# Performance work log

Measured on AMD Instinct MI355X. Metric: run time of the kernel, lower is better.

## Reference

```python
import jax, jax.numpy as jnp
import numpy as np

NUM_HEADS = 16


def setup_inputs() -> dict:
    key = jax.random.key(0)
    ks = jax.random.split(key, 7)
    B, S, D = 2, 2048, 1024
    return {
        "query": jax.random.normal(ks[0], (B, S, D), jnp.float32),
        "key": jax.random.normal(ks[1], (B, S, D), jnp.float32),
        "value": jax.random.normal(ks[2], (B, S, D), jnp.float32),
        "qk_w": jax.random.normal(ks[3], (2 * D, D), jnp.float32) * (D ** -0.5),
        "qk_b": jax.random.normal(ks[4], (2 * D,), jnp.float32) * 0.02,
        "out_w": jax.random.normal(ks[5], (D, D), jnp.float32) * (D ** -0.5),
        "out_b": jax.random.normal(ks[6], (D,), jnp.float32) * 0.02,
    }


def reference(query, key, value, qk_w, qk_b, out_w, out_b):
    # Hand-rolled multi-head attention with fused QK projection (both Q and K
    # come from `query`); `key` arg is unused (as in the source forward).
    B, S, D = query.shape
    H = NUM_HEADS
    dh = D // H
    scale = D ** -0.5  # source uses d_model**-0.5, not head_dim

    qk = query @ qk_w.T + qk_b                      # [B, S, 2D]
    qk = qk.reshape(B, S, 2, H, dh).transpose(2, 0, 3, 1, 4)  # [2, B, H, S, dh]
    q, k = qk[0], qk[1]                              # [B, H, S, dh]

    scores = jnp.einsum("bhqd,bhkd->bhqk", q, k) * scale  # [B, H, S, S]
    attn = jax.nn.softmax(scores, axis=-1)
    # dropout_p = 0.0 -> identity (eval mode)

    v = value.reshape(B, S, H, dh).transpose(0, 2, 1, 3)   # [B, H, S, dh]
    out = jnp.einsum("bhqk,bhkd->bhqd", attn, v)           # [B, H, S, dh]
    out = out.transpose(0, 2, 1, 3).reshape(B, S, D)       # merge heads
    return out @ out_w.T + out_b
```

## Files before the change

kernel.cpp:

```cpp
#include <hip/hip_runtime.h>
#include <hip/hip_bf16.h>
#include <stdint.h>

typedef __attribute__((ext_vector_type(8))) short bf16x8;
typedef __attribute__((ext_vector_type(4))) short bf16x4;
typedef __attribute__((ext_vector_type(4))) float f32x4;
typedef __attribute__((ext_vector_type(16))) float f32x16;

#define B_ 2
#define H_ 16
#define S_ 2048
#define D_ 1024
#define DH 64

__device__ __forceinline__ void gload_lds16(const void* g, void* l) {
  __builtin_amdgcn_global_load_lds((const __attribute__((address_space(1))) void*)g,
                                   (__attribute__((address_space(3))) void*)l, 16, 0, 0);
}

__device__ __forceinline__ float exp2_hw(float x) {
  float r;
  asm("v_exp_f32 %0, %1" : "=v"(r) : "v"(x));
  return r;
}

__device__ __forceinline__ uint32_t packbf2(float lo, float hi) {
  union { __hip_bfloat162 h; uint32_t u; } u;
  u.h = __float22bfloat162_rn(make_float2(lo, hi));
  return u.u;
}

__device__ __forceinline__ void pl32swap(uint32_t& a, uint32_t& b) {
  asm volatile("v_permlane32_swap_b32 %0, %1" : "+v"(a), "+v"(b));
}

__global__ void k_f2b(const float* __restrict__ in, __hip_bfloat16* __restrict__ out, int n8) {
  int i = blockIdx.x * blockDim.x + threadIdx.x;
  if (i >= n8) return;
  const float4* p = (const float4*)in + (size_t)i * 2;
  float4 a = p[0], b = p[1];
  union { bf16x8 v; __hip_bfloat16 h[8]; } u;
  u.h[0] = __float2bfloat16(a.x); u.h[1] = __float2bfloat16(a.y);
  u.h[2] = __float2bfloat16(a.z); u.h[3] = __float2bfloat16(a.w);
  u.h[4] = __float2bfloat16(b.x); u.h[5] = __float2bfloat16(b.y);
  u.h[6] = __float2bfloat16(b.z); u.h[7] = __float2bfloat16(b.w);
  *((bf16x8*)out + i) = u.v;
}

__global__ void k_vt(const float* __restrict__ v, __hip_bfloat16* __restrict__ vt) {
  __shared__ float tile[64][65];
  const int bh = blockIdx.y, b = bh >> 4, h = bh & 15;
  const int s0 = blockIdx.x * 64;
  const int t = threadIdx.x;
#pragma unroll
  for (int it = 0; it < 4; ++it) {
    const int r = it * 16 + (t >> 4);
    const int c = (t & 15) * 4;
    const float4 x = *(const float4*)(v + (size_t)(b * S_ + s0 + r) * D_ + h * DH + c);
    tile[r][c] = x.x; tile[r][c + 1] = x.y; tile[r][c + 2] = x.z; tile[r][c + 3] = x.w;
  }
  __syncthreads();
#pragma unroll
  for (int it = 0; it < 4; ++it) {
    const int d = it * 16 + (t >> 4);
    const int j = (t & 15) * 4;
    union { bf16x4 v4; __hip_bfloat16 e[4]; } u;
    u.e[0] = __float2bfloat16(tile[j][d]);
    u.e[1] = __float2bfloat16(tile[j + 1][d]);
    u.e[2] = __float2bfloat16(tile[j + 2][d]);
    u.e[3] = __float2bfloat16(tile[j + 3][d]);
    *(bf16x4*)(vt + (size_t)(bh * DH + d) * S_ + s0 + j) = u.v4;
  }
}

__device__ __forceinline__ void gemm_tile_128(
    const __hip_bfloat16* __restrict__ A, const __hip_bfloat16* __restrict__ Bm,
    int K, int m0, int n0, __hip_bfloat16* As, __hip_bfloat16* Bs, f32x4 acc[4][4]) {
  const int t = threadIdx.x;
  const int l = t & 63, w = t >> 6;
  const int wr = w >> 1, wc = w & 1;
  const int lr = l & 15, lc = l >> 4;
  const int srow = t >> 2;
  const int sbyte = ((t & 3) << 4) ^ ((srow & 3) << 4);
  const char* AsB = (const char*)As;
  const char* BsB = (const char*)Bs;
  const int aswz = (lc << 4) ^ ((lr & 3) << 4);
  const size_t rowK = (size_t)K;
  const __hip_bfloat16* gA0 = A + (size_t)(m0 + srow) * rowK + (sbyte >> 1);
  const __hip_bfloat16* gB0 = Bm + (size_t)(n0 + srow) * rowK + (sbyte >> 1);
  for (int k0 = 0; k0 < K; k0 += 32) {
    __syncthreads();
    gload_lds16(gA0 + k0, (void*)&As[t * 8]);
    gload_lds16(gA0 + 64 * rowK + k0, (void*)&As[(256 + t) * 8]);
    gload_lds16(gB0 + k0, (void*)&Bs[t * 8]);
    gload_lds16(gB0 + 64 * rowK + k0, (void*)&Bs[(256 + t) * 8]);
    __syncthreads();
    bf16x8 af[4], bfr[4];
#pragma unroll
    for (int i = 0; i < 4; ++i)
      af[i] = *(const bf16x8*)(AsB + (wr * 64 + i * 16 + lr) * 64 + aswz);
#pragma unroll
    for (int j = 0; j < 4; ++j)
      bfr[j] = *(const bf16x8*)(BsB + (wc * 64 + j * 16 + lr) * 64 + aswz);
#pragma unroll
    for (int i = 0; i < 4; ++i)
#pragma unroll
      for (int j = 0; j < 4; ++j)
        acc[i][j] = __builtin_amdgcn_mfma_f32_16x16x32_bf16(af[i], bfr[j], acc[i][j], 0, 0, 0);
  }
}

__global__ __launch_bounds__(256) void k_gemm_qk(
    const __hip_bfloat16* __restrict__ A, const __hip_bfloat16* __restrict__ Bm,
    const float* __restrict__ bias,
    __hip_bfloat16* __restrict__ Qh, __hip_bfloat16* __restrict__ Kh) {
  __shared__ __align__(16) __hip_bfloat16 As[128 * 32];
  __shared__ __align__(16) __hip_bfloat16 Bs[128 * 32];
  f32x4 acc[4][4] = {};
  const int m0 = blockIdx.x * 128, n0 = blockIdx.y * 128;
  gemm_tile_128(A, Bm, 1024, m0, n0, As, Bs, acc);
  const int t = threadIdx.x, l = t & 63, w = t >> 6;
  const int wr = w >> 1, wc = w & 1, lr = l & 15, lc = l >> 4;
#pragma unroll
  for (int j = 0; j < 4; ++j) {
    const int col = n0 + wc * 64 + j * 16 + lr;
    const float bv = bias[col];
    const int inK = col >> 10;
    const int hh = (col & 1023) >> 6, dd = col & 63;
    __hip_bfloat16* dst = inK ? Kh : Qh;
    const float sc = inK ? 1.0f : 0.045084220f;
#pragma unroll
    for (int i = 0; i < 4; ++i) {
#pragma unroll
      for (int r = 0; r < 4; ++r) {
        const int row = m0 + wr * 64 + i * 16 + lc * 4 + r;
        const int b = row >> 11, s = row & 2047;
        const float vv = (acc[i][j][r] + bv) * sc;
        dst[((size_t)(b * H_ + hh) * S_ + s) * DH + dd] = __float2bfloat16(vv);
      }
    }
  }
}

__global__ __launch_bounds__(256) void k_gemm_out(
    const __hip_bfloat16* __restrict__ A, const __hip_bfloat16* __restrict__ Bm,
    const float* __restrict__ bias, float* __restrict__ out) {
  __shared__ __align__(16) __hip_bfloat16 As[128 * 32];
  __shared__ __align__(16) __hip_bfloat16 Bs[128 * 32];
  f32x4 acc[4][4] = {};
  const int m0 = blockIdx.x * 128, n0 = blockIdx.y * 128;
  gemm_tile_128(A, Bm, 1024, m0, n0, As, Bs, acc);
  const int t = threadIdx.x, l = t & 63, w = t >> 6;
  const int wr = w >> 1, wc = w & 1, lr = l & 15, lc = l >> 4;
#pragma unroll
  for (int j = 0; j < 4; ++j) {
    const int col = n0 + wc * 64 + j * 16 + lr;
    const float bv = bias[col];
#pragma unroll
    for (int i = 0; i < 4; ++i) {
#pragma unroll
      for (int r = 0; r < 4; ++r) {
        const int row = m0 + wr * 64 + i * 16 + lc * 4 + r;
        out[(size_t)row * D_ + col] = acc[i][j][r] + bv;
      }
    }
  }
}

__global__ __launch_bounds__(256) void k_attn(
    const __hip_bfloat16* __restrict__ Qh, const __hip_bfloat16* __restrict__ Kh,
    const __hip_bfloat16* __restrict__ VT, __hip_bfloat16* __restrict__ attO) {
  __shared__ __align__(16) __hip_bfloat16 KV[2][8192];
  __shared__ float fbuf[4][32];
  const int bh = blockIdx.y, q0 = blockIdx.x * 128;
  const int t = threadIdx.x, l = t & 63, w = t >> 6;
  const int qi = l & 31, hi = l >> 5;
  const __hip_bfloat16* Qb = Qh + (size_t)bh * S_ * DH;
  const __hip_bfloat16* Kb = Kh + (size_t)bh * S_ * DH;
  const __hip_bfloat16* Vb = VT + (size_t)bh * DH * S_;

  bf16x8 qf[4];
#pragma unroll
  for (int dc = 0; dc < 4; ++dc)
    qf[dc] = *(const bf16x8*)&Qb[(size_t)(q0 + w * 32 + qi) * DH + dc * 16 + hi * 8];

  const int tr = t >> 4, tc = t & 15;
  const int c0 = tc ^ (tr & 15);
  const int c1 = tc ^ ((tr + 16) & 15);
  const __hip_bfloat16* gK0 = Kb + (size_t)(tr + (c0 >= 8 ? 32 : 0)) * DH + (c0 & 7) * 8;
  const __hip_bfloat16* gK1 = Kb + (size_t)(tr + 16 + (c1 >= 8 ? 32 : 0)) * DH + (c1 & 7) * 8;
  const __hip_bfloat16* gV0 = Vb + (size_t)(tr + (c0 >= 8 ? 32 : 0)) * S_ + (c0 & 7) * 8;
  const __hip_bfloat16* gV1 = Vb + (size_t)(tr + 16 + (c1 >= 8 ? 32 : 0)) * S_ + (c1 & 7) * 8;

#define STAGE(bufi, j0)                                              \
  {                                                                  \
    __hip_bfloat16* Ld = &KV[bufi][0];                               \
    gload_lds16(gK0 + (size_t)(j0) * DH, Ld + t * 8);                \
    gload_lds16(gK1 + (size_t)(j0) * DH, Ld + 2048 + t * 8);         \
    gload_lds16(gV0 + (j0), Ld + 4096 + t * 8);                      \
    gload_lds16(gV1 + (j0), Ld + 4096 + 2048 + t * 8);               \
  }

  f32x16 oacc0 = {}, oacc1 = {};
  float m = -1e30f, lsum = 0.f;
  int buf = 0;

  STAGE(0, 0)
  __syncthreads();

  const int rsw = (qi & 15) << 4;

  for (int j0 = 0; j0 < S_; j0 += 64) {
    if (j0 + 64 < S_) STAGE(buf ^ 1, j0 + 64)
    const char* KsB = (const char*)&KV[buf][0];
    const char* VsB = (const char*)&KV[buf][4096];

    f32x16 s0 = {}, s1 = {};
#pragma unroll
    for (int dc = 0; dc < 4; ++dc) {
      const int cb = dc * 32 + hi * 16;
      const bf16x8 kf0 = *(const bf16x8*)(KsB + qi * 256 + (cb ^ rsw));
      const bf16x8 kf1 = *(const bf16x8*)(KsB + qi * 256 + ((128 + cb) ^ rsw));
      s0 = __builtin_amdgcn_mfma_f32_32x32x16_bf16(kf0, qf[dc], s0, 0, 0, 0);
      s1 = __builtin_amdgcn_mfma_f32_32x32x16_bf16(kf1, qf[dc], s1, 0, 0, 0);
    }

    float pm = -1e30f;
#pragma unroll
    for (int r = 0; r < 16; ++r) pm = fmaxf(pm, fmaxf(s0[r], s1[r]));
    pm = fmaxf(pm, __shfl_xor(pm, 32, 64));
    if (!__all(pm <= m + 8.0f)) {
      const float mn = fmaxf(m, pm);
      const float al = exp2_hw(m - mn);
      if (l < 32) fbuf[w][l] = al;
      asm volatile("s_waitcnt lgkmcnt(0)" ::: "memory");
#pragma unroll
      for (int r = 0; r < 16; ++r) {
        const float ar = fbuf[w][(r & 3) + 8 * (r >> 2) + 4 * hi];
        oacc0[r] *= ar;
        oacc1[r] *= ar;
      }
      lsum *= al;
      m = mn;
    }
    float rs = 0.f;
#pragma unroll
    for (int r = 0; r < 16; ++r) { s0[r] = exp2_hw(s0[r] - m); rs += s0[r]; }
#pragma unroll
    for (int r = 0; r < 16; ++r) { s1[r] = exp2_hw(s1[r] - m); rs += s1[r]; }
    rs += __shfl_xor(rs, 32, 64);
    lsum += rs;

#define PVSTEP(SS, KSOFF)                                                         \
  {                                                                               \
    uint32_t w0 = packbf2(SS[0], SS[1]), w1 = packbf2(SS[2], SS[3]);              \
    uint32_t w2 = packbf2(SS[4], SS[5]), w3 = packbf2(SS[6], SS[7]);              \
    uint32_t w4 = packbf2(SS[8], SS[9]), w5 = packbf2(SS[10], SS[11]);            \
    uint32_t w6 = packbf2(SS[12], SS[13]), w7 = packbf2(SS[14], SS[15]);          \
    pl32swap(w0, w2); pl32swap(w1, w3); pl32swap(w4, w6); pl32swap(w5, w7);       \
    union { bf16x8 v; uint32_t u[4]; } pa0, pa1;                                  \
    pa0.u[0] = w0; pa0.u[1] = w1; pa0.u[2] = w2; pa0.u[3] = w3;                   \
    pa1.u[0] = w4; pa1.u[1] = w5; pa1.u[2] = w6; pa1.u[3] = w7;                   \
    const int cb = (KSOFF) + hi * 16;                                             \
    bf16x8 vf;                                                                    \
    vf = *(const bf16x8*)(VsB + qi * 256 + ((cb + 0) ^ rsw));                     \
    oacc0 = __builtin_amdgcn_mfma_f32_32x32x16_bf16(pa0.v, vf, oacc0, 0, 0, 0);   \
    vf = *(const bf16x8*)(VsB + qi * 256 + ((cb + 32) ^ rsw));                    \
    oacc0 = __builtin_amdgcn_mfma_f32_32x32x16_bf16(pa1.v, vf, oacc0, 0, 0, 0);   \
    vf = *(const bf16x8*)(VsB + qi * 256 + ((cb + 128) ^ rsw));                   \
    oacc1 = __builtin_amdgcn_mfma_f32_32x32x16_bf16(pa0.v, vf, oacc1, 0, 0, 0);   \
    vf = *(const bf16x8*)(VsB + qi * 256 + ((cb + 128 + 32) ^ rsw));              \
    oacc1 = __builtin_amdgcn_mfma_f32_32x32x16_bf16(pa1.v, vf, oacc1, 0, 0, 0);   \
  }
    PVSTEP(s0, 0)
    PVSTEP(s1, 64)

    __syncthreads();
    buf ^= 1;
  }

  if (l < 32) fbuf[w][l] = lsum;
  asm volatile("s_waitcnt lgkmcnt(0)" ::: "memory");
  const int b = bh >> 4, h = bh & 15;
#pragma unroll
  for (int r = 0; r < 16; ++r) {
    const int qloc = (r & 3) + 8 * (r >> 2) + 4 * hi;
    const float inv = 1.0f / fbuf[w][qloc];
    const size_t base = ((size_t)(b * S_) + q0 + w * 32 + qloc) * D_ + h * DH;
    attO[base + qi] = __float2bfloat16(oacc0[r] * inv);
    attO[base + 32 + qi] = __float2bfloat16(oacc1[r] * inv);
  }
#undef STAGE
#undef PVSTEP
}

extern "C" void kernel_launch(void* const* d_in, const int* in_sizes, int n_in,
                              void* d_out, int out_size, void* d_ws, size_t ws_size,
                              hipStream_t stream) {
  const float* q   = (const float*)d_in[0];
  const float* val = (const float*)d_in[2];
  const float* qkw = (const float*)d_in[3];
  const float* qkb = (const float*)d_in[4];
  const float* ow  = (const float*)d_in[5];
  const float* ob  = (const float*)d_in[6];
  float* out = (float*)d_out;

  __hip_bfloat16* ws  = (__hip_bfloat16*)d_ws;
  __hip_bfloat16* qA  = ws;
  __hip_bfloat16* w1b = qA + 4194304;
  __hip_bfloat16* w2b = w1b + 2097152;
  __hip_bfloat16* Qh  = w2b + 1048576;
  __hip_bfloat16* Kh  = Qh + 4194304;
  __hip_bfloat16* VT  = Kh + 4194304;
  __hip_bfloat16* aO  = VT + 4194304;

  hipLaunchKernelGGL(k_f2b, dim3(2048), dim3(256), 0, stream, q, qA, 524288);
  hipLaunchKernelGGL(k_f2b, dim3(1024), dim3(256), 0, stream, qkw, w1b, 262144);
  hipLaunchKernelGGL(k_f2b, dim3(512), dim3(256), 0, stream, ow, w2b, 131072);
  hipLaunchKernelGGL(k_vt, dim3(32, 32), dim3(256), 0, stream, val, VT);
  hipLaunchKernelGGL(k_gemm_qk, dim3(32, 16), dim3(256), 0, stream, qA, w1b, qkb, Qh, Kh);
  hipLaunchKernelGGL(k_attn, dim3(16, 32), dim3(256), 0, stream, Qh, Kh, VT, aO);
  hipLaunchKernelGGL(k_gemm_out, dim3(32, 8), dim3(256), 0, stream, aO, w2b, ob, out);
}
```

Measured before the change: 132.8 us.

## Split attention KV range across two blocks with combine pass; fuse conversion kernels

The three fp32-to-bf16 conversion launches are merged into one kernel. Attention is split along the key dimension into two halves (flash-decoding style), doubling the grid from 512 to 1024 blocks to improve CU occupancy on the 256-CU part. A new combine kernel merges the two partial outputs using their saved max and sum values. The attention kernel also adds s_setprio around the MFMA sections, tree reductions for row max and sum, and a launch bound of 4. The cost is an extra launch and extra partial-output traffic, and the partials are rounded to bf16 before combining.

```diff
diff --git a/kernel.cpp b/kernel.cpp
--- a/kernel.cpp
+++ b/kernel.cpp
@@ -34,17 +34,24 @@
   asm volatile("v_permlane32_swap_b32 %0, %1" : "+v"(a), "+v"(b));
 }
 
-__global__ void k_f2b(const float* __restrict__ in, __hip_bfloat16* __restrict__ out, int n8) {
+__global__ void k_f2b3(const float* __restrict__ a, __hip_bfloat16* __restrict__ da,
+                       const float* __restrict__ b, __hip_bfloat16* __restrict__ db,
+                       const float* __restrict__ c, __hip_bfloat16* __restrict__ dc) {
   int i = blockIdx.x * blockDim.x + threadIdx.x;
-  if (i >= n8) return;
-  const float4* p = (const float4*)in + (size_t)i * 2;
-  float4 a = p[0], b = p[1];
+  const float* src;
+  __hip_bfloat16* dst;
+  int off;
+  if (i < 524288) { src = a; dst = da; off = i; }
+  else if (i < 786432) { src = b; dst = db; off = i - 524288; }
+  else { src = c; dst = dc; off = i - 786432; }
+  const float4* p = (const float4*)src + (size_t)off * 2;
+  float4 x = p[0], y = p[1];
   union { bf16x8 v; __hip_bfloat16 h[8]; } u;
-  u.h[0] = __float2bfloat16(a.x); u.h[1] = __float2bfloat16(a.y);
-  u.h[2] = __float2bfloat16(a.z); u.h[3] = __float2bfloat16(a.w);
-  u.h[4] = __float2bfloat16(b.x); u.h[5] = __float2bfloat16(b.y);
-  u.h[6] = __float2bfloat16(b.z); u.h[7] = __float2bfloat16(b.w);
-  *((bf16x8*)out + i) = u.v;
+  u.h[0] = __float2bfloat16(x.x); u.h[1] = __float2bfloat16(x.y);
+  u.h[2] = __float2bfloat16(x.z); u.h[3] = __float2bfloat16(x.w);
+  u.h[4] = __float2bfloat16(y.x); u.h[5] = __float2bfloat16(y.y);
+  u.h[6] = __float2bfloat16(y.z); u.h[7] = __float2bfloat16(y.w);
+  *((bf16x8*)dst + off) = u.v;
 }
 
 __global__ void k_vt(const float* __restrict__ v, __hip_bfloat16* __restrict__ vt) {
@@ -167,12 +174,16 @@
   }
 }
 
-__global__ __launch_bounds__(256) void k_attn(
+__global__ __launch_bounds__(256, 4) void k_attn(
     const __hip_bfloat16* __restrict__ Qh, const __hip_bfloat16* __restrict__ Kh,
-    const __hip_bfloat16* __restrict__ VT, __hip_bfloat16* __restrict__ attO) {
+    const __hip_bfloat16* __restrict__ VT,
+    __hip_bfloat16* __restrict__ pO0, __hip_bfloat16* __restrict__ pO1,
+    float2* __restrict__ ml0, float2* __restrict__ ml1) {
   __shared__ __align__(16) __hip_bfloat16 KV[2][8192];
   __shared__ float fbuf[4][32];
   const int bh = blockIdx.y, q0 = blockIdx.x * 128;
+  const int half = blockIdx.z;
+  const int jbeg = half << 10, jend = jbeg + 1024;
   const int t = threadIdx.x, l = t & 63, w = t >> 6;
   const int qi = l & 31, hi = l >> 5;
   const __hip_bfloat16* Qb = Qh + (size_t)bh * S_ * DH;
@@ -205,17 +216,18 @@
   float m = -1e30f, lsum = 0.f;
   int buf = 0;
 
-  STAGE(0, 0)
+  STAGE(0, jbeg)
   __syncthreads();
 
   const int rsw = (qi & 15) << 4;
 
-  for (int j0 = 0; j0 < S_; j0 += 64) {
-    if (j0 + 64 < S_) STAGE(buf ^ 1, j0 + 64)
+  for (int j0 = jbeg; j0 < jend; j0 += 64) {
+    if (j0 + 64 < jend) STAGE(buf ^ 1, j0 + 64)
     const char* KsB = (const char*)&KV[buf][0];
     const char* VsB = (const char*)&KV[buf][4096];
 
     f32x16 s0 = {}, s1 = {};
+    __builtin_amdgcn_s_setprio(1);
 #pragma unroll
     for (int dc = 0; dc < 4; ++dc) {
       const int cb = dc * 32 + hi * 16;
@@ -224,11 +236,16 @@
       s0 = __builtin_amdgcn_mfma_f32_32x32x16_bf16(kf0, qf[dc], s0, 0, 0, 0);
       s1 = __builtin_amdgcn_mfma_f32_32x32x16_bf16(kf1, qf[dc], s1, 0, 0, 0);
     }
-
-    float pm = -1e30f;
-#pragma unroll
-    for (int r = 0; r < 16; ++r) pm = fmaxf(pm, fmaxf(s0[r], s1[r]));
-    pm = fmaxf(pm, __shfl_xor(pm, 32, 64));
+    __builtin_amdgcn_s_setprio(0);
+
+    float tm[16];
+#pragma unroll
+    for (int r = 0; r < 16; ++r) tm[r] = fmaxf(s0[r], s1[r]);
+#pragma unroll
+    for (int st = 8; st > 0; st >>= 1)
+#pragma unroll
+      for (int r = 0; r < st; ++r) tm[r] = fmaxf(tm[r], tm[r + st]);
+    float pm = fmaxf(tm[0], __shfl_xor(tm[0], 32, 64));
     if (!__all(pm <= m + 8.0f)) {
       const float mn = fmaxf(m, pm);
       const float al = exp2_hw(m - mn);
@@ -243,13 +260,18 @@
       lsum *= al;
       m = mn;
     }
-    float rs = 0.f;
-#pragma unroll
-    for (int r = 0; r < 16; ++r) { s0[r] = exp2_hw(s0[r] - m); rs += s0[r]; }
-#pragma unroll
-    for (int r = 0; r < 16; ++r) { s1[r] = exp2_hw(s1[r] - m); rs += s1[r]; }
-    rs += __shfl_xor(rs, 32, 64);
-    lsum += rs;
+#pragma unroll
+    for (int r = 0; r < 16; ++r) s0[r] = exp2_hw(s0[r] - m);
+#pragma unroll
+    for (int r = 0; r < 16; ++r) s1[r] = exp2_hw(s1[r] - m);
+    float ts[16];
+#pragma unroll
+    for (int r = 0; r < 16; ++r) ts[r] = s0[r] + s1[r];
+#pragma unroll
+    for (int st = 8; st > 0; st >>= 1)
+#pragma unroll
+      for (int r = 0; r < st; ++r) ts[r] += ts[r + st];
+    lsum += ts[0] + __shfl_xor(ts[0], 32, 64);
 
 #define PVSTEP(SS, KSOFF)                                                         \
   {                                                                               \
@@ -272,26 +294,52 @@
     vf = *(const bf16x8*)(VsB + qi * 256 + ((cb + 128 + 32) ^ rsw));              \
     oacc1 = __builtin_amdgcn_mfma_f32_32x32x16_bf16(pa1.v, vf, oacc1, 0, 0, 0);   \
   }
+    __builtin_amdgcn_s_setprio(1);
     PVSTEP(s0, 0)
     PVSTEP(s1, 64)
+    __builtin_amdgcn_s_setprio(0);
 
     __syncthreads();
     buf ^= 1;
   }
 
-  if (l < 32) fbuf[w][l] = lsum;
-  asm volatile("s_waitcnt lgkmcnt(0)" ::: "memory");
-  const int b = bh >> 4, h = bh & 15;
+  __hip_bfloat16* pO = half ? pO1 : pO0;
+  float2* ml = half ? ml1 : ml0;
+  const size_t rowb = (size_t)bh * S_ + q0 + w * 32;
 #pragma unroll
   for (int r = 0; r < 16; ++r) {
     const int qloc = (r & 3) + 8 * (r >> 2) + 4 * hi;
-    const float inv = 1.0f / fbuf[w][qloc];
-    const size_t base = ((size_t)(b * S_) + q0 + w * 32 + qloc) * D_ + h * DH;
-    attO[base + qi] = __float2bfloat16(oacc0[r] * inv);
-    attO[base + 32 + qi] = __float2bfloat16(oacc1[r] * inv);
-  }
+    pO[(rowb + qloc) * 64 + qi] = __float2bfloat16(oacc0[r]);
+    pO[(rowb + qloc) * 64 + 32 + qi] = __float2bfloat16(oacc1[r]);
+  }
+  if (l < 32) ml[rowb + qi] = make_float2(m, lsum);
 #undef STAGE
 #undef PVSTEP
+}
+
+__global__ __launch_bounds__(256) void k_combine(
+    const __hip_bfloat16* __restrict__ pO0, const __hip_bfloat16* __restrict__ pO1,
+    const float2* __restrict__ ml0, const float2* __restrict__ ml1,
+    __hip_bfloat16* __restrict__ aO) {
+  const int tid = blockIdx.x * 256 + threadIdx.x;
+  const float2 a = ml0[tid], b = ml1[tid];
+  const float M = fmaxf(a.x, b.x);
+  const float w0 = exp2_hw(a.x - M), w1 = exp2_hw(b.x - M);
+  const float inv = 1.0f / (w0 * a.y + w1 * b.y);
+  const float c0 = w0 * inv, c1 = w1 * inv;
+  const bf16x8* r0 = (const bf16x8*)(pO0 + (size_t)tid * 64);
+  const bf16x8* r1 = (const bf16x8*)(pO1 + (size_t)tid * 64);
+  const int bh = tid >> 11, s = tid & 2047, bb = bh >> 4, h = bh & 15;
+  __hip_bfloat16* o = aO + ((size_t)(bb * S_ + s)) * D_ + h * DH;
+#pragma unroll
+  for (int j = 0; j < 8; ++j) {
+    union { bf16x8 v; __hip_bfloat16 e[8]; } v0, v1, u;
+    v0.v = r0[j]; v1.v = r1[j];
+#pragma unroll
+    for (int e = 0; e < 8; ++e)
+      u.e[e] = __float2bfloat16(c0 * __bfloat162float(v0.e[e]) + c1 * __bfloat162float(v1.e[e]));
+    *(bf16x8*)(o + j * 8) = u.v;
+  }
 }
 
 extern "C" void kernel_launch(void* const* d_in, const int* in_sizes, int n_in,
@@ -313,12 +361,15 @@
   __hip_bfloat16* Kh  = Qh + 4194304;
   __hip_bfloat16* VT  = Kh + 4194304;
   __hip_bfloat16* aO  = VT + 4194304;
-
-  hipLaunchKernelGGL(k_f2b, dim3(2048), dim3(256), 0, stream, q, qA, 524288);
-  hipLaunchKernelGGL(k_f2b, dim3(1024), dim3(256), 0, stream, qkw, w1b, 262144);
-  hipLaunchKernelGGL(k_f2b, dim3(512), dim3(256), 0, stream, ow, w2b, 131072);
+  __hip_bfloat16* pO1 = aO + 4194304;
+  __hip_bfloat16* pO0 = qA;
+  float2* ml0 = (float2*)w1b;
+  float2* ml1 = ml0 + 65536;
+
+  hipLaunchKernelGGL(k_f2b3, dim3(3584), dim3(256), 0, stream, q, qA, qkw, w1b, ow, w2b);
   hipLaunchKernelGGL(k_vt, dim3(32, 32), dim3(256), 0, stream, val, VT);
   hipLaunchKernelGGL(k_gemm_qk, dim3(32, 16), dim3(256), 0, stream, qA, w1b, qkb, Qh, Kh);
-  hipLaunchKernelGGL(k_attn, dim3(16, 32), dim3(256), 0, stream, Qh, Kh, VT, aO);
+  hipLaunchKernelGGL(k_attn, dim3(16, 32, 2), dim3(256), 0, stream, Qh, Kh, VT, pO0, pO1, ml0, ml1);
+  hipLaunchKernelGGL(k_combine, dim3(256), dim3(256), 0, stream, pO0, pO1, ml0, ml1, aO);
   hipLaunchKernelGGL(k_gemm_out, dim3(32, 8), dim3(256), 0, stream, aO, w2b, ob, out);
 }
```

Measured after the change: 132.5 us. Within noise of the previous version (-0.3%).
